# Kernel optimization log

Hardware: AMD Instinct MI355X
Metric: run time of the kernel (lower is better)

The kernel has to match this reference:

```python
import jax, jax.numpy as jnp
import numpy as np

D = 1024
B, S = 4, 2048

def setup_inputs() -> dict:
    key = jax.random.key(0)
    ks = jax.random.split(key, 9)
    scale = 1.0 / np.sqrt(D)
    return {
        "queries": jax.random.normal(ks[0], (B, S, D), dtype=jnp.float32),
        "keys": jax.random.normal(ks[1], (B, S, D), dtype=jnp.float32),
        "values": jax.random.normal(ks[2], (B, S, D), dtype=jnp.float32),
        # torch nn.Linear weights: [out, in], y = x @ W.T + b
        "Wq": jax.random.uniform(ks[3], (D, D), jnp.float32, -scale, scale),
        "bq": jax.random.uniform(ks[4], (D,), jnp.float32, -scale, scale),
        "Wk": jax.random.uniform(ks[5], (D, D), jnp.float32, -scale, scale),
        "bk": jax.random.uniform(ks[6], (D,), jnp.float32, -scale, scale),
        "Wv": jax.random.uniform(ks[7], (D, D), jnp.float32, -scale, scale),
        "bv": jax.random.uniform(ks[8], (D,), jnp.float32, -scale, scale),
    }

def reference(queries, keys, values, Wq, bq, Wk, bk, Wv, bv):
    # Linear projections (torch convention: x @ W.T + b)
    Q = jnp.einsum('bsd,ed->bse', queries, Wq) + bq  # [B,S,D]
    K = jnp.einsum('bsd,ed->bse', keys, Wk) + bk
    V = jnp.einsum('bsd,ed->bse', values, Wv) + bv
    # relu attention: no softmax, no scaling (faithful to source)
    scores = jax.nn.relu(jnp.einsum('bqd,bkd->bqk', Q, K))  # [B,S,S]
    return jnp.einsum('bqk,bkd->bqd', scores, V)
```

## Files before the change

kernel.cpp:

```cpp
#include <hip/hip_runtime.h>
#include <hip/hip_bf16.h>
#include <stdint.h>

typedef __bf16 bf16_t;
typedef __bf16 bf16x8 __attribute__((ext_vector_type(8)));
typedef float  f32x4  __attribute__((ext_vector_type(4)));

__device__ __forceinline__ void async_copy16(const bf16_t* g, bf16_t* l) {
    __builtin_amdgcn_global_load_lds(
        (const __attribute__((address_space(1))) unsigned int*)(uintptr_t)g,
        (__attribute__((address_space(3))) unsigned int*)(uintptr_t)l,
        16, 0, 0);
}

#define BARR()  asm volatile("s_barrier" ::: "memory")
#define VMW(n)  asm volatile("s_waitcnt vmcnt(" #n ")" ::: "memory")


#define STAGEA(buf, h, kt) do {                                                   \
    _Pragma("unroll") for (int j = 0; j < 2; j++)                                 \
        async_copy16(ApM + (long)(h)*128*K + (long)(kt)*64 + offJ[j],             \
                     (bf16_t*)(lds + (buf)*65536 + (h)*16384 + ldst_[j]));        \
} while (0)

#define STAGEB(buf, h, kt) do {                                                   \
    _Pragma("unroll") for (int j = 0; j < 2; j++)                                 \
        async_copy16(BpN + (long)(h)*128*K + (long)(kt)*64 + offJ[j],             \
                     (bf16_t*)(lds + (buf)*65536 + 32768 + (h)*16384 + ldst_[j]));\
} while (0)

#define LOADA(buf, hA) do {                                                       \
    _Pragma("unroll") for (int m = 0; m < 4; m++)                                 \
    _Pragma("unroll") for (int ks = 0; ks < 2; ks++) {                            \
        const int R = (hA)*128 + sr*64 + m*16 + l15;                              \
        afr[m][ks] = *(const bf16x8*)(lds + (buf)*65536 + R*128                   \
                                      + (((ks*4 + l4) ^ (l15 & 7)) << 4));        \
    } } while (0)

#define LOADB(buf, hB) do {                                                       \
    _Pragma("unroll") for (int n = 0; n < 2; n++)                                 \
    _Pragma("unroll") for (int ks = 0; ks < 2; ks++) {                            \
        const int Cc = (hB)*128 + sc*32 + n*16 + l15;                             \
        bfr[hB][n][ks] = *(const bf16x8*)(lds + (buf)*65536 + 32768 + Cc*128      \
                                          + (((ks*4 + l4) ^ (l15 & 7)) << 4));    \
    } } while (0)

#define MMA(hA, hB) do {                                                          \
    __builtin_amdgcn_s_setprio(1);                                                \
    _Pragma("unroll") for (int m = 0; m < 4; m++)                                 \
    _Pragma("unroll") for (int n = 0; n < 2; n++)                                 \
    _Pragma("unroll") for (int ks = 0; ks < 2; ks++)                              \
        acc[hA][hB][m][n] = __builtin_amdgcn_mfma_f32_16x16x32_bf16(              \
            afr[m][ks], bfr[hB][n][ks], acc[hA][hB][m][n], 0, 0, 0);              \
    __builtin_amdgcn_s_setprio(0);                                                \
} while (0)

template<bool OUT_F32, bool RELU, int BIAS_MODE>
__global__ __launch_bounds__(512, 2)
void gemm256(const bf16_t* __restrict__ A, const bf16_t* __restrict__ B,
             const float* __restrict__ bias, void* __restrict__ Cp,
             int K, int ldc, long sAb, long sBb, long sCb)
{
    __shared__ char lds[131072];

    const int gx = gridDim.x, gy = gridDim.y;
    const int tot = gx * gy * gridDim.z;
    const int lin = (blockIdx.z * gy + blockIdx.y) * gx + blockIdx.x;
    const int q8  = tot >> 3;
    const int wg  = (lin & 7) * q8 + (lin >> 3);
    const int bz  = wg / (gx * gy);
    const int r2  = wg - bz * gx * gy;
    const int by  = r2 / gx;
    const int bx  = r2 - by * gx;
    const int blockM = by * 256;
    const int blockN = bx * 256;

    const int t    = threadIdx.x;
    const int lane = t & 63;
    const int wave = t >> 6;
    const int sr   = wave >> 2;
    const int sc   = wave & 3;
    const int l15  = lane & 15;
    const int l4   = lane >> 4;

    const bf16_t* Ab  = A + sAb * (long)bz;
    const bf16_t* Bb  = B + sBb * (long)bz;
    const bf16_t* ApM = Ab + (long)blockM * K;
    const bf16_t* BpN = Bb + (long)blockN * K;

    long     offJ[2];
    uint32_t ldst_[2];
    #pragma unroll
    for (int j = 0; j < 2; j++) {
        const int c = t + j * 512;
        const int r = c >> 3, s = c & 7;
        offJ[j]  = (long)r * K + ((s ^ (r & 7)) * 8);
        ldst_[j] = (uint32_t)c * 16;
    }

    f32x4  acc[2][2][4][2] = {};
    bf16x8 afr[4][2];
    bf16x8 bfr[2][2][2];

    const int NT = K >> 6;
    const int NI = NT >> 1;

    STAGEA(0, 0, 0); STAGEB(0, 0, 0); STAGEA(0, 1, 0); STAGEB(0, 1, 0);
    STAGEA(1, 0, 1); STAGEB(1, 0, 1);
    VMW(4);
    BARR();

    for (int i = 0; i < NI; ++i) {
        const int  T    = 2 * i;
        const bool last = (i == NI - 1);

        LOADA(0, 0); LOADB(0, 0);
        STAGEA(1, 1, T + 1);
        BARR();
        MMA(0, 0);
        VMW(6);
        BARR();
        LOADB(0, 1);
        STAGEB(1, 1, T + 1);
        BARR();
        MMA(0, 1);
        BARR();
        LOADA(0, 1);
        if (!last) STAGEA(0, 0, T + 2);
        BARR();
        MMA(1, 0);
        BARR();
        if (!last) STAGEB(0, 0, T + 2);
        BARR();
        MMA(1, 1);
        if (last) { VMW(0); } else { VMW(6); }
        BARR();
        LOADA(1, 0); LOADB(1, 0);
        if (!last) STAGEA(0, 1, T + 2);
        BARR();
        MMA(0, 0);
        if (!last) VMW(6);
        BARR();
        LOADB(1, 1);
        if (!last) STAGEB(0, 1, T + 2);
        BARR();
        MMA(0, 1);
        BARR();
        LOADA(1, 1);
        if (!last) STAGEA(1, 0, T + 3);
        BARR();
        MMA(1, 0);
        BARR();
        if (!last) STAGEB(1, 0, T + 3);
        BARR();
        MMA(1, 1);
        if (!last) VMW(6);
        BARR();
    }

    float*  Cf = (float*) Cp + sCb * (long)bz;
    bf16_t* Ch = (bf16_t*)Cp + sCb * (long)bz;
    #pragma unroll
    for (int hA = 0; hA < 2; hA++)
    #pragma unroll
    for (int hB = 0; hB < 2; hB++)
    #pragma unroll
    for (int m = 0; m < 4; m++)
    #pragma unroll
    for (int n = 0; n < 2; n++) {
        const int gcol = blockN + hB * 128 + sc * 32 + n * 16 + l15;
        float bc = 0.f;
        if (BIAS_MODE == 1) bc = bias[gcol];
        #pragma unroll
        for (int reg = 0; reg < 4; reg++) {
            const int grow = blockM + hA * 128 + sr * 64 + m * 16 + l4 * 4 + reg;
            float vv = acc[hA][hB][m][n][reg];
            if (BIAS_MODE == 1) vv += bc;
            if (BIAS_MODE == 2) vv += bias[grow];
            if (RELU) vv = fmaxf(vv, 0.f);
            if (OUT_F32) Cf[(long)grow * ldc + gcol] = vv;
            else         Ch[(long)grow * ldc + gcol] = (bf16_t)vv;
        }
    }
}

__global__ __launch_bounds__(256)
void cast_all_kernel(const float* __restrict__ q, const float* __restrict__ k,
                     const float* __restrict__ v, const float* __restrict__ Wq,
                     const float* __restrict__ Wk, const float* __restrict__ Wv,
                     bf16_t* __restrict__ ws)
{
    const long BIG = 1048576;
    const long SMALL = 131072;
    long id = (long)blockIdx.x * blockDim.x + threadIdx.x;
    const float* src; bf16_t* dst;
    if (id < 3 * BIG) {
        int s = (int)(id / BIG);
        long off = (id - (long)s * BIG) * 8;
        src = (s == 0 ? q : s == 1 ? k : v) + off;
        dst = ws + (long)s * 8388608 + off;
    } else {
        long id2 = id - 3 * BIG;
        int s = (int)(id2 / SMALL);
        long off = (id2 - (long)s * SMALL) * 8;
        src = (s == 0 ? Wq : s == 1 ? Wk : Wv) + off;
        dst = ws + 25165824L + (long)s * 1048576 + off;
    }
    float4 v0 = ((const float4*)src)[0];
    float4 v1 = ((const float4*)src)[1];
    alignas(16) bf16_t o[8];
    o[0]=(bf16_t)v0.x; o[1]=(bf16_t)v0.y; o[2]=(bf16_t)v0.z; o[3]=(bf16_t)v0.w;
    o[4]=(bf16_t)v1.x; o[5]=(bf16_t)v1.y; o[6]=(bf16_t)v1.z; o[7]=(bf16_t)v1.w;
    *(uint4*)dst = *(const uint4*)o;
}

extern "C" void kernel_launch(void* const* d_in, const int* in_sizes, int n_in,
                              void* d_out, int out_size, void* d_ws, size_t ws_size,
                              hipStream_t stream)
{
    const float* q   = (const float*)d_in[0];
    const float* k   = (const float*)d_in[1];
    const float* v   = (const float*)d_in[2];
    const float* Wq  = (const float*)d_in[3];
    const float* bq  = (const float*)d_in[4];
    const float* Wk  = (const float*)d_in[5];
    const float* bk  = (const float*)d_in[6];
    const float* Wv  = (const float*)d_in[7];
    const float* bv  = (const float*)d_in[8];

    const int B = 4, S = 2048, D = 1024;

    bf16_t* ws  = (bf16_t*)d_ws;
    bf16_t* qb  = ws;
    bf16_t* kb  = ws + 8388608L;
    bf16_t* vb  = ws + 16777216L;
    bf16_t* Wqb = ws + 25165824L;
    bf16_t* Wkb = ws + 26214400L;
    bf16_t* Wvb = ws + 27262976L;
    bf16_t* Qp  = ws + 28311552L;
    bf16_t* Kp  = ws + 36700160L;
    bf16_t* VpT = ws + 45088768L;
    bf16_t* Sc  = ws;

    cast_all_kernel<<<dim3(13824), dim3(256), 0, stream>>>(q, k, v, Wq, Wk, Wv, ws);

    dim3 blk(512);

    gemm256<false, false, 1><<<dim3(4, 32, 1), blk, 0, stream>>>(
        qb, Wqb, bq, Qp, D, D, 0L, 0L, 0L);

    gemm256<false, false, 1><<<dim3(4, 32, 1), blk, 0, stream>>>(
        kb, Wkb, bk, Kp, D, D, 0L, 0L, 0L);

    gemm256<false, false, 2><<<dim3(8, 4, 4), blk, 0, stream>>>(
        Wvb, vb, bv, VpT, D, S, 0L, (long)S * D, (long)D * S);

    gemm256<false, true, 0><<<dim3(8, 8, 4), blk, 0, stream>>>(
        Qp, Kp, nullptr, Sc, D, S, (long)S * D, (long)S * D, (long)S * S);

    gemm256<true, false, 0><<<dim3(4, 8, 4), blk, 0, stream>>>(
        Sc, VpT, nullptr, d_out, S, D, (long)S * S, (long)D * S, (long)S * D);
}
```

Measured before the change: 326.5 us.

## Switch GEMM to 32x32x16 MFMA, merge Q/K projections, use BM=128 for small grids

```diff
diff --git a/kernel.cpp b/kernel.cpp
--- a/kernel.cpp
+++ b/kernel.cpp
@@ -4,7 +4,7 @@
 
 typedef __bf16 bf16_t;
 typedef __bf16 bf16x8 __attribute__((ext_vector_type(8)));
-typedef float  f32x4  __attribute__((ext_vector_type(4)));
+typedef float  f32x16 __attribute__((ext_vector_type(16)));
 
 __device__ __forceinline__ void async_copy16(const bf16_t* g, bf16_t* l) {
     __builtin_amdgcn_global_load_lds(
@@ -13,55 +13,65 @@
         16, 0, 0);
 }
 
-#define BARR()  asm volatile("s_barrier" ::: "memory")
-#define VMW(n)  asm volatile("s_waitcnt vmcnt(" #n ")" ::: "memory")
+template<int N> __device__ __forceinline__ void vmw() {
+    if constexpr (N == 0)      asm volatile("s_waitcnt vmcnt(0)");
+    else if constexpr (N == 5) asm volatile("s_waitcnt vmcnt(5)");
+    else if constexpr (N == 6) asm volatile("s_waitcnt vmcnt(6)");
+}
+#define BARR() __builtin_amdgcn_s_barrier()
 
 
 #define STAGEA(buf, h, kt) do {                                                   \
-    _Pragma("unroll") for (int j = 0; j < 2; j++)                                 \
-        async_copy16(ApM + (long)(h)*128*K + (long)(kt)*64 + offJ[j],             \
-                     (bf16_t*)(lds + (buf)*65536 + (h)*16384 + ldst_[j]));        \
+    _Pragma("unroll") for (int j = 0; j < LA; j++)                                \
+        async_copy16(ApM + (long)(h)*(BM/2)*K + (long)(kt)*64 + offA[j],          \
+                     (bf16_t*)(lds + (buf)*BUF + (h)*HBYTES + dstA[j]));          \
 } while (0)
 
 #define STAGEB(buf, h, kt) do {                                                   \
     _Pragma("unroll") for (int j = 0; j < 2; j++)                                 \
-        async_copy16(BpN + (long)(h)*128*K + (long)(kt)*64 + offJ[j],             \
-                     (bf16_t*)(lds + (buf)*65536 + 32768 + (h)*16384 + ldst_[j]));\
+        async_copy16(BpN + (long)(h)*128*K + (long)(kt)*64 + offB[j],             \
+                     (bf16_t*)(lds + (buf)*BUF + ABYTES + (h)*16384 + dstB[j]));  \
 } while (0)
 
 #define LOADA(buf, hA) do {                                                       \
-    _Pragma("unroll") for (int m = 0; m < 4; m++)                                 \
-    _Pragma("unroll") for (int ks = 0; ks < 2; ks++) {                            \
-        const int R = (hA)*128 + sr*64 + m*16 + l15;                              \
-        afr[m][ks] = *(const bf16x8*)(lds + (buf)*65536 + R*128                   \
-                                      + (((ks*4 + l4) ^ (l15 & 7)) << 4));        \
+    _Pragma("unroll") for (int m = 0; m < MT; m++)                                \
+    _Pragma("unroll") for (int ks = 0; ks < 4; ks++) {                            \
+        const int R = (hA)*(BM/2) + sr*(BM/4) + m*32 + r32;                       \
+        af[m][ks] = *(const bf16x8*)(lds + (buf)*BUF + R*128                      \
+                                     + (((ks*2 + half) ^ (R & 7)) << 4));         \
     } } while (0)
 
 #define LOADB(buf, hB) do {                                                       \
-    _Pragma("unroll") for (int n = 0; n < 2; n++)                                 \
-    _Pragma("unroll") for (int ks = 0; ks < 2; ks++) {                            \
-        const int Cc = (hB)*128 + sc*32 + n*16 + l15;                             \
-        bfr[hB][n][ks] = *(const bf16x8*)(lds + (buf)*65536 + 32768 + Cc*128      \
-                                          + (((ks*4 + l4) ^ (l15 & 7)) << 4));    \
+    _Pragma("unroll") for (int ks = 0; ks < 4; ks++) {                            \
+        const int Cc = (hB)*128 + sc*32 + r32;                                    \
+        bf[hB][ks] = *(const bf16x8*)(lds + (buf)*BUF + ABYTES + Cc*128           \
+                                      + (((ks*2 + half) ^ (Cc & 7)) << 4));       \
     } } while (0)
 
 #define MMA(hA, hB) do {                                                          \
     __builtin_amdgcn_s_setprio(1);                                                \
-    _Pragma("unroll") for (int m = 0; m < 4; m++)                                 \
-    _Pragma("unroll") for (int n = 0; n < 2; n++)                                 \
-    _Pragma("unroll") for (int ks = 0; ks < 2; ks++)                              \
-        acc[hA][hB][m][n] = __builtin_amdgcn_mfma_f32_16x16x32_bf16(              \
-            afr[m][ks], bfr[hB][n][ks], acc[hA][hB][m][n], 0, 0, 0);              \
+    _Pragma("unroll") for (int m = 0; m < MT; m++)                                \
+    _Pragma("unroll") for (int ks = 0; ks < 4; ks++)                              \
+        acc[hA][hB][m] = __builtin_amdgcn_mfma_f32_32x32x16_bf16(                 \
+            af[m][ks], bf[hB][ks], acc[hA][hB][m], 0, 0, 0);                      \
     __builtin_amdgcn_s_setprio(0);                                                \
 } while (0)
 
-template<bool OUT_F32, bool RELU, int BIAS_MODE>
+template<int BM, bool OUT_F32, bool RELU, int BIAS_MODE, bool BIAS_SPLIT>
 __global__ __launch_bounds__(512, 2)
 void gemm256(const bf16_t* __restrict__ A, const bf16_t* __restrict__ B,
-             const float* __restrict__ bias, void* __restrict__ Cp,
+             const float* __restrict__ bias0, const float* __restrict__ bias1,
+             void* __restrict__ Cp,
              int K, int ldc, long sAb, long sBb, long sCb)
 {
-    __shared__ char lds[131072];
+    constexpr int MT     = BM / 128;
+    constexpr int LA     = BM / 128;
+    constexpr int VMN    = 4 + LA;
+    constexpr int ABYTES = BM * 128;
+    constexpr int HBYTES = ABYTES / 2;
+    constexpr int BUF    = ABYTES + 32768;
+
+    __shared__ char lds[2 * BUF];
 
     const int gx = gridDim.x, gy = gridDim.y;
     const int tot = gx * gy * gridDim.z;
@@ -72,7 +82,7 @@
     const int r2  = wg - bz * gx * gy;
     const int by  = r2 / gx;
     const int bx  = r2 - by * gx;
-    const int blockM = by * 256;
+    const int blockM = by * BM;
     const int blockN = bx * 256;
 
     const int t    = threadIdx.x;
@@ -80,101 +90,104 @@
     const int wave = t >> 6;
     const int sr   = wave >> 2;
     const int sc   = wave & 3;
-    const int l15  = lane & 15;
-    const int l4   = lane >> 4;
-
-    const bf16_t* Ab  = A + sAb * (long)bz;
-    const bf16_t* Bb  = B + sBb * (long)bz;
-    const bf16_t* ApM = Ab + (long)blockM * K;
-    const bf16_t* BpN = Bb + (long)blockN * K;
-
-    long     offJ[2];
-    uint32_t ldst_[2];
+    const int r32  = lane & 31;
+    const int half = lane >> 5;
+
+    const bf16_t* ApM = A + sAb * (long)bz + (long)blockM * K;
+    const bf16_t* BpN = B + sBb * (long)bz + (long)blockN * K;
+
+    long offA[LA]; uint32_t dstA[LA];
+    #pragma unroll
+    for (int j = 0; j < LA; j++) {
+        const int c = t + j * 512, r = c >> 3, s = c & 7;
+        offA[j] = (long)r * K + ((s ^ (r & 7)) * 8);
+        dstA[j] = (uint32_t)c * 16;
+    }
+    long offB[2]; uint32_t dstB[2];
     #pragma unroll
     for (int j = 0; j < 2; j++) {
-        const int c = t + j * 512;
-        const int r = c >> 3, s = c & 7;
-        offJ[j]  = (long)r * K + ((s ^ (r & 7)) * 8);
-        ldst_[j] = (uint32_t)c * 16;
-    }
-
-    f32x4  acc[2][2][4][2] = {};
-    bf16x8 afr[4][2];
-    bf16x8 bfr[2][2][2];
+        const int c = t + j * 512, r = c >> 3, s = c & 7;
+        offB[j] = (long)r * K + ((s ^ (r & 7)) * 8);
+        dstB[j] = (uint32_t)c * 16;
+    }
+
+    f32x16 acc[2][2][MT] = {};
+    bf16x8 af[MT][4];
+    bf16x8 bf[2][4];
 
     const int NT = K >> 6;
     const int NI = NT >> 1;
 
-    STAGEA(0, 0, 0); STAGEB(0, 0, 0); STAGEA(0, 1, 0); STAGEB(0, 1, 0);
-    STAGEA(1, 0, 1); STAGEB(1, 0, 1);
-    VMW(4);
+    STAGEA(0, 0, 0); STAGEB(0, 0, 0); STAGEB(0, 1, 0); STAGEA(0, 1, 0);
+    STAGEA(1, 0, 1); STAGEB(1, 0, 1); STAGEB(1, 1, 1);
+    vmw<VMN>();
     BARR();
 
     for (int i = 0; i < NI; ++i) {
-        const int  T    = 2 * i;
-        const bool last = (i == NI - 1);
+        const int  T  = 2 * i;
+        const bool nl = (i < NI - 1);
 
         LOADA(0, 0); LOADB(0, 0);
         STAGEA(1, 1, T + 1);
+        if constexpr (MT == 2) asm volatile("s_waitcnt lgkmcnt(8)");
         BARR();
         MMA(0, 0);
-        VMW(6);
         BARR();
         LOADB(0, 1);
-        STAGEB(1, 1, T + 1);
+        if (nl) STAGEA(0, 0, T + 2);
         BARR();
         MMA(0, 1);
         BARR();
         LOADA(0, 1);
-        if (!last) STAGEA(0, 0, T + 2);
+        if (nl) STAGEB(0, 0, T + 2);
         BARR();
         MMA(1, 0);
         BARR();
-        if (!last) STAGEB(0, 0, T + 2);
+        if (nl) STAGEB(0, 1, T + 2);
         BARR();
         MMA(1, 1);
-        if (last) { VMW(0); } else { VMW(6); }
+        if (nl) vmw<VMN>(); else vmw<0>();
         BARR();
         LOADA(1, 0); LOADB(1, 0);
-        if (!last) STAGEA(0, 1, T + 2);
+        if (nl) STAGEA(0, 1, T + 2);
+        if constexpr (MT == 2) asm volatile("s_waitcnt lgkmcnt(8)");
         BARR();
         MMA(0, 0);
-        if (!last) VMW(6);
         BARR();
         LOADB(1, 1);
-        if (!last) STAGEB(0, 1, T + 2);
+        if (nl) STAGEA(1, 0, T + 3);
         BARR();
         MMA(0, 1);
         BARR();
         LOADA(1, 1);
-        if (!last) STAGEA(1, 0, T + 3);
+        if (nl) STAGEB(1, 0, T + 3);
         BARR();
         MMA(1, 0);
         BARR();
-        if (!last) STAGEB(1, 0, T + 3);
+        if (nl) STAGEB(1, 1, T + 3);
         BARR();
         MMA(1, 1);
-        if (!last) VMW(6);
+        if (nl) vmw<VMN>();
         BARR();
     }
 
     float*  Cf = (float*) Cp + sCb * (long)bz;
     bf16_t* Ch = (bf16_t*)Cp + sCb * (long)bz;
+    const float* bias = (BIAS_SPLIT && bz) ? bias1 : bias0;
     #pragma unroll
     for (int hA = 0; hA < 2; hA++)
     #pragma unroll
     for (int hB = 0; hB < 2; hB++)
     #pragma unroll
-    for (int m = 0; m < 4; m++)
-    #pragma unroll
-    for (int n = 0; n < 2; n++) {
-        const int gcol = blockN + hB * 128 + sc * 32 + n * 16 + l15;
+    for (int m = 0; m < MT; m++) {
+        const int gcol = blockN + hB * 128 + sc * 32 + r32;
         float bc = 0.f;
         if (BIAS_MODE == 1) bc = bias[gcol];
         #pragma unroll
-        for (int reg = 0; reg < 4; reg++) {
-            const int grow = blockM + hA * 128 + sr * 64 + m * 16 + l4 * 4 + reg;
-            float vv = acc[hA][hB][m][n][reg];
+        for (int reg = 0; reg < 16; reg++) {
+            const int grow = blockM + hA * (BM / 2) + sr * (BM / 4) + m * 32
+                           + (reg & 3) + 8 * (reg >> 2) + 4 * half;
+            float vv = acc[hA][hB][m][reg];
             if (BIAS_MODE == 1) vv += bc;
             if (BIAS_MODE == 2) vv += bias[grow];
             if (RELU) vv = fmaxf(vv, 0.f);
@@ -228,17 +241,14 @@
     const float* Wv  = (const float*)d_in[7];
     const float* bv  = (const float*)d_in[8];
 
-    const int B = 4, S = 2048, D = 1024;
+    const int S = 2048, D = 1024;
 
     bf16_t* ws  = (bf16_t*)d_ws;
     bf16_t* qb  = ws;
-    bf16_t* kb  = ws + 8388608L;
     bf16_t* vb  = ws + 16777216L;
     bf16_t* Wqb = ws + 25165824L;
-    bf16_t* Wkb = ws + 26214400L;
     bf16_t* Wvb = ws + 27262976L;
     bf16_t* Qp  = ws + 28311552L;
-    bf16_t* Kp  = ws + 36700160L;
     bf16_t* VpT = ws + 45088768L;
     bf16_t* Sc  = ws;
 
@@ -246,18 +256,17 @@
 
     dim3 blk(512);
 
-    gemm256<false, false, 1><<<dim3(4, 32, 1), blk, 0, stream>>>(
-        qb, Wqb, bq, Qp, D, D, 0L, 0L, 0L);
-
-    gemm256<false, false, 1><<<dim3(4, 32, 1), blk, 0, stream>>>(
-        kb, Wkb, bk, Kp, D, D, 0L, 0L, 0L);
-
-    gemm256<false, false, 2><<<dim3(8, 4, 4), blk, 0, stream>>>(
-        Wvb, vb, bv, VpT, D, S, 0L, (long)S * D, (long)D * S);
-
-    gemm256<false, true, 0><<<dim3(8, 8, 4), blk, 0, stream>>>(
-        Qp, Kp, nullptr, Sc, D, S, (long)S * D, (long)S * D, (long)S * S);
-
-    gemm256<true, false, 0><<<dim3(4, 8, 4), blk, 0, stream>>>(
-        Sc, VpT, nullptr, d_out, S, D, (long)S * S, (long)D * S, (long)S * D);
-}
+    gemm256<256, false, false, 1, true><<<dim3(4, 32, 2), blk, 0, stream>>>(
+        qb, Wqb, bq, bk, Qp, D, D, 8388608L, 1048576L, 8388608L);
+
+    gemm256<128, false, false, 2, false><<<dim3(8, 8, 4), blk, 0, stream>>>(
+        Wvb, vb, bv, nullptr, VpT, D, S, 0L, (long)S * D, (long)D * S);
+
+    gemm256<256, false, true, 0, false><<<dim3(8, 8, 4), blk, 0, stream>>>(
+        Qp, Qp + 8388608L, nullptr, nullptr, Sc, D, S,
+        (long)S * D, (long)S * D, (long)S * S);
+
+    gemm256<128, true, false, 0, false><<<dim3(4, 16, 4), blk, 0, stream>>>(
+        Sc, VpT, nullptr, nullptr, d_out, S, D,
+        (long)S * S, (long)D * S, (long)S * D);
+}
```

Measured after the change: 294.9 us. 1.11x faster.
